# Optimization experiments

Hardware: AMD Instinct MI355X
Metric: run time of the kernel (lower is better)

## Reference

```python
import jax, jax.numpy as jnp
import numpy as np

T, OBS, H, NOBJ = 32768, 256, 512, 4


def _xavier(key, shape):
    fan_in, fan_out = shape[0], shape[1]
    lim = jnp.sqrt(6.0 / (fan_in + fan_out)).astype(jnp.float32)
    return jax.random.uniform(key, shape, jnp.float32, -lim, lim)


def setup_inputs() -> dict:
    key = jax.random.key(0)
    ks = jax.random.split(key, 16)
    # weights stored as [in, out] so y = x @ W (same math as nn.Linear with W.T)
    return {
        "x": jax.random.normal(ks[0], (T, OBS), jnp.float32),
        "W_in0": _xavier(ks[1], (OBS, H)),
        "W_B0": _xavier(ks[2], (OBS, H)),
        "W_C0": _xavier(ks[3], (OBS, H)),
        "W_d0": _xavier(ks[4], (OBS, H)),
        "A_log0": jax.random.normal(ks[5], (H,), jnp.float32),
        "W_in1": _xavier(ks[6], (H, H)),
        "W_B1": _xavier(ks[7], (H, H)),
        "W_C1": _xavier(ks[8], (H, H)),
        "W_d1": _xavier(ks[9], (H, H)),
        "A_log1": jax.random.normal(ks[10], (H,), jnp.float32),
        "W_out": _xavier(ks[11], (H, NOBJ)),
        "b_out": jnp.zeros((NOBJ,), jnp.float32),
        "W_skip": _xavier(ks[12], (OBS, NOBJ)),
    }


def _mamba_layer(x, W_in, W_B, W_C, W_d, A_log):
    # x: [T, D_in] -> [T, H]
    x_state = x @ W_in           # [T, H]
    B = x @ W_B                  # [T, H]
    C = x @ W_C                  # [T, H]
    delta = jax.nn.sigmoid(x @ W_d)  # [T, H]
    A = -jnp.exp(A_log)          # [H]
    A_bar = jnp.exp(delta * A)   # [T, H], in (0, 1)
    Bx = B * x_state             # [T, H]

    def step(h, inp):
        a_t, bx_t = inp
        h = a_t * h + bx_t
        return h, h

    h0 = jnp.zeros((x_state.shape[-1],), x_state.dtype)
    _, h_seq = jax.lax.scan(step, h0, (A_bar, Bx))  # [T, H]
    return C * h_seq


def reference(x, W_in0, W_B0, W_C0, W_d0, A_log0,
              W_in1, W_B1, W_C1, W_d1, A_log1,
              W_out, b_out, W_skip):
    skip = x
    y = _mamba_layer(x, W_in0, W_B0, W_C0, W_d0, A_log0)
    y = _mamba_layer(y, W_in1, W_B1, W_C1, W_d1, A_log1)
    out = y @ W_out + b_out + skip @ W_skip  # [T, NOBJ]
    return out
```

## Files before the change

### kernel.cpp

```cpp
#include <hip/hip_runtime.h>

typedef __attribute__((ext_vector_type(8))) short short8;
typedef __attribute__((ext_vector_type(4))) float floatx4;

#define T_SIZE 32768
#define OBS    256
#define H      512
#define NC     1024
#define CHUNK  32
#define NGRP   64
#define GCH    16
#define SLAB   ((size_t)T_SIZE * 32)

__device__ __forceinline__ unsigned short f2bf(float f){
    union { float f; unsigned u; } v; v.f = f;
    unsigned u = v.u;
    u += 0x7FFFu + ((u >> 16) & 1u);
    return (unsigned short)(u >> 16);
}
__device__ __forceinline__ float bf2f(unsigned short u){
    union { unsigned u; float f; } v; v.u = ((unsigned)u) << 16; return v.f;
}

#define GLOAD_LDS16(g, l) \
    __builtin_amdgcn_global_load_lds((const __attribute__((address_space(1))) unsigned*)(g), \
                                     (__attribute__((address_space(3))) unsigned*)(l), 16, 0, 0)

__global__ void cast_x_kernel(const float* __restrict__ x, unsigned short* __restrict__ xb, int n4){
    int i = blockIdx.x * 256 + threadIdx.x;
    if (i < n4){
        float4 v = ((const float4*)x)[i];
        ushort4 o;
        o.x = f2bf(v.x); o.y = f2bf(v.y); o.z = f2bf(v.z); o.w = f2bf(v.w);
        ((ushort4*)xb)[i] = o;
    }
}

__global__ void tcast4_kernel(const float* __restrict__ W0, const float* __restrict__ W1,
                              const float* __restrict__ W2, const float* __restrict__ W3,
                              unsigned short* __restrict__ dst, int K, int KH){
    int idx = blockIdx.x * 256 + threadIdx.x;
    if (idx >= 4 * KH) return;
    int s   = idx / KH;
    int rem = idx - s * KH;
    int k = rem >> 9;
    int h = rem & 511;
    const float* W = (s == 0) ? W0 : (s == 1) ? W1 : (s == 2) ? W2 : W3;
    int b = h >> 4, hh = h & 15;
    dst[(size_t)((b * 4 + s) * 16 + hh) * K + k] = f2bf(W[(size_t)k * H + h]);
}

template<int K>
__global__ __launch_bounds__(512, 2) void gemm_layer_kernel(
    const unsigned short* __restrict__ xb,
    const unsigned short* __restrict__ wt,
    const float* __restrict__ A_log,
    unsigned short* __restrict__ gT, unsigned short* __restrict__ bxT, unsigned short* __restrict__ CT,
    float* __restrict__ Pbuf, float* __restrict__ Hbuf)
{
    __shared__ unsigned short SM[4][16384];

    const int tid  = threadIdx.x;
    const int wave = tid >> 6;
    const int lane = tid & 63;
    const int ml   = lane & 15;
    const int quad = lane >> 4;
    const int wm   = wave >> 2;
    const int wn   = wave & 3;

    const int flat = blockIdx.y * 8 + blockIdx.x;
    const int xcd  = flat & 7;
    const int j    = flat >> 3;
    const int nb   = j & 7;
    const int mb   = (j >> 3) * 8 + xcd;
    const int m0   = mb * 256;

    const int srow = tid >> 2;
    const int sel  = ((tid & 3) ^ ((tid >> 3) & 3)) * 8;
    const int swz  = (ml >> 1) & 3;

    const unsigned short* pa0 = xb + (size_t)(m0 + srow) * K + sel;
    const unsigned short* pa1 = pa0 + (size_t)128 * K;
    const unsigned short* pb0 = wt + (size_t)(nb * 256 + srow) * K + sel;
    const unsigned short* pb1 = pb0 + (size_t)128 * K;

    const int ldsA0 = wave * 512;
    const int ldsA1 = 4096  + wave * 512;
    const int ldsB0 = 8192  + wave * 512;
    const int ldsB1 = 12288 + wave * 512;

    const int rbaseA = (wm * 128 + ml) * 32 + (quad ^ swz) * 8;
    const int rbaseB = (wn * 64  + ml) * 32 + (quad ^ swz) * 8;

    floatx4 acc[8][4];
    #pragma unroll
    for (int m = 0; m < 8; m++)
        #pragma unroll
        for (int n = 0; n < 4; n++)
            acc[m][n] = (floatx4)(0.0f);

    constexpr int NK = K >> 5;

#define STAGE_A(kt_) { const int b_ = (kt_) & 3; const int ko_ = (kt_) * 32; \
        GLOAD_LDS16(pa0 + ko_, &SM[b_][ldsA0]); \
        GLOAD_LDS16(pa1 + ko_, &SM[b_][ldsA1]); }
#define STAGE_B(kt_) { const int b_ = (kt_) & 3; const int ko_ = (kt_) * 32; \
        GLOAD_LDS16(pb0 + ko_, &SM[b_][ldsB0]); \
        GLOAD_LDS16(pb1 + ko_, &SM[b_][ldsB1]); }

    STAGE_A(0); STAGE_B(0);
    STAGE_A(1); STAGE_B(1);
    STAGE_A(2); STAGE_B(2);
    asm volatile("s_waitcnt vmcnt(8)" ::: "memory");
    __builtin_amdgcn_s_barrier();
    __builtin_amdgcn_sched_barrier(0);

    #pragma unroll
    for (int kt = 0; kt < NK; ++kt){
        const unsigned short* SA = &SM[kt & 3][0];
        const unsigned short* SB = SA + 8192;

        short8 av[4], bv[4];
        #pragma unroll
        for (int m = 0; m < 4; m++) av[m] = *(const short8*)(SA + rbaseA + m * 512);
        #pragma unroll
        for (int n = 0; n < 4; n++) bv[n] = *(const short8*)(SB + rbaseB + n * 512);
        if (kt + 3 < NK) STAGE_A(kt + 3);
        __builtin_amdgcn_s_barrier();
        asm volatile("s_waitcnt lgkmcnt(0)" ::: "memory");
        __builtin_amdgcn_sched_barrier(0);
        __builtin_amdgcn_s_setprio(1);
        #pragma unroll
        for (int m = 0; m < 4; m++)
            #pragma unroll
            for (int n = 0; n < 4; n++)
                acc[m][n] = __builtin_amdgcn_mfma_f32_16x16x32_bf16(av[m], bv[n], acc[m][n], 0, 0, 0);
        __builtin_amdgcn_s_setprio(0);
        __builtin_amdgcn_s_barrier();
        __builtin_amdgcn_sched_barrier(0);

        short8 aw[4];
        #pragma unroll
        for (int m = 0; m < 4; m++) aw[m] = *(const short8*)(SA + rbaseA + (m + 4) * 512);
        if (kt + 3 < NK) STAGE_B(kt + 3);
        __builtin_amdgcn_s_barrier();
        asm volatile("s_waitcnt lgkmcnt(0)" ::: "memory");
        __builtin_amdgcn_sched_barrier(0);
        __builtin_amdgcn_s_setprio(1);
        #pragma unroll
        for (int m = 0; m < 4; m++)
            #pragma unroll
            for (int n = 0; n < 4; n++)
                acc[m + 4][n] = __builtin_amdgcn_mfma_f32_16x16x32_bf16(aw[m], bv[n], acc[m + 4][n], 0, 0, 0);
        __builtin_amdgcn_s_setprio(0);
        if (kt + 1 < NK){
            if (kt + 3 < NK)       { asm volatile("s_waitcnt vmcnt(8)" ::: "memory"); }
            else if (kt + 3 == NK) { asm volatile("s_waitcnt vmcnt(4)" ::: "memory"); }
            else                   { asm volatile("s_waitcnt vmcnt(0)" ::: "memory"); }
        }
        __builtin_amdgcn_s_barrier();
        __builtin_amdgcn_sched_barrier(0);
    }
    __syncthreads();

#undef STAGE_A
#undef STAGE_B

    unsigned short* SMe = &SM[0][0];
    float2* segbuf = (float2*)(SMe + 49152);
    const int hcol  = wn * 16 + ml;
    const int hb    = wn >> 1;
    const int col32 = (wn & 1) * 16 + ml;
    const float Aneg = -expf(A_log[(nb * 4 + wn) * 16 + ml]);

    #pragma unroll
    for (int m = 0; m < 8; m++){
        float p = 1.0f, hh = 0.0f;
        #pragma unroll
        for (int r = 0; r < 4; r++){
            int trow = wm * 128 + m * 16 + quad * 4 + r;
            float dv = acc[m][3][r];
            float delta = 1.0f / (1.0f + expf(-dv));
            unsigned short gb = f2bf(delta * Aneg);
            float a = expf(bf2f(gb));
            unsigned short bb = f2bf(acc[m][1][r] * acc[m][0][r]);
            int base = hb * 8192 + trow * 32 + col32;
            SMe[        base] = gb;
            SMe[16384 + base] = bb;
            SMe[32768 + base] = f2bf(acc[m][2][r]);
            hh = fmaf(a, hh, bf2f(bb));
            p *= a;
        }
        const int ch = wm * 4 + (m >> 1);
        const int s  = (m & 1) * 4 + quad;
        segbuf[(ch * 8 + s) * 64 + hcol] = make_float2(p, hh);
    }
    __syncthreads();
    {
        const short8* s8 = (const short8*)SMe;
        #pragma unroll
        for (int arr = 0; arr < 3; arr++){
            unsigned short* bp = (arr == 0) ? gT : (arr == 1) ? bxT : CT;
            #pragma unroll
            for (int h2 = 0; h2 < 2; h2++){
                short8* d = (short8*)(bp + (size_t)(nb * 2 + h2) * SLAB + (size_t)m0 * 32);
                d[tid]       = s8[arr * 2048 + h2 * 1024 + tid];
                d[tid + 512] = s8[arr * 2048 + h2 * 1024 + tid + 512];
            }
        }
    }
    {
        const int ccol = tid & 63, ch = tid >> 6;
        float P = 1.0f, Hc = 0.0f;
        #pragma unroll
        for (int s = 0; s < 8; s++){
            float2 ph = segbuf[(ch * 8 + s) * 64 + ccol];
            Hc = fmaf(ph.x, Hc, ph.y);
            P *= ph.x;
        }
        const int c = mb * 8 + ch;
        Pbuf[(size_t)c * H + nb * 64 + ccol] = P;
        Hbuf[(size_t)c * H + nb * 64 + ccol] = Hc;
    }
}

__global__ void scan2a_kernel(const float* __restrict__ P, const float* __restrict__ Hc,
                              float* __restrict__ Pg, float* __restrict__ Hg){
    const int g  = blockIdx.x;
    const int j4 = threadIdx.x * 4;
    float4 pc = {1.f,1.f,1.f,1.f}, hc = {0.f,0.f,0.f,0.f};
    #pragma unroll
    for (int i = 0; i < GCH; i++){
        size_t o = (size_t)(g * GCH + i) * H + j4;
        float4 P4 = *(const float4*)(P + o);
        float4 H4 = *(const float4*)(Hc + o);
        hc.x = fmaf(P4.x, hc.x, H4.x); pc.x *= P4.x;
        hc.y = fmaf(P4.y, hc.y, H4.y); pc.y *= P4.y;
        hc.z = fmaf(P4.z, hc.z, H4.z); pc.z *= P4.z;
        hc.w = fmaf(P4.w, hc.w, H4.w); pc.w *= P4.w;
    }
    *(float4*)(Pg + (size_t)g * H + j4) = pc;
    *(float4*)(Hg + (size_t)g * H + j4) = hc;
}

__global__ void scan2b_kernel(const float* __restrict__ Pg, const float* __restrict__ Hg,
                              float* __restrict__ Cg){
    const int j = threadIdx.x;
    float carry = 0.0f;
    for (int g0 = 0; g0 < NGRP; g0 += 8){
        float p[8], h[8];
        #pragma unroll
        for (int i = 0; i < 8; i++){
            p[i] = Pg[(size_t)(g0 + i) * H + j];
            h[i] = Hg[(size_t)(g0 + i) * H + j];
        }
        #pragma unroll
        for (int i = 0; i < 8; i++){
            Cg[(size_t)(g0 + i) * H + j] = carry;
            carry = fmaf(p[i], carry, h[i]);
        }
    }
}

__global__ void scan3_kernel(const unsigned short* __restrict__ gT, const unsigned short* __restrict__ bxT,
                             const unsigned short* __restrict__ CT,
                             const float* __restrict__ P, const float* __restrict__ Hc,
                             const float* __restrict__ Cg,
                             unsigned short* __restrict__ yb){
    int idx = blockIdx.x * 256 + threadIdx.x;
    int j4 = (idx & 127) * 4;
    int c  = idx >> 7;
    int nb = j4 >> 5, jj = j4 & 31;
    int grp = c >> 4;
    float4 h = *(const float4*)(Cg + (size_t)grp * H + j4);
    for (int cc = grp << 4; cc < c; ++cc){
        float4 P4 = *(const float4*)(P + (size_t)cc * H + j4);
        float4 H4 = *(const float4*)(Hc + (size_t)cc * H + j4);
        h.x = fmaf(P4.x, h.x, H4.x);
        h.y = fmaf(P4.y, h.y, H4.y);
        h.z = fmaf(P4.z, h.z, H4.z);
        h.w = fmaf(P4.w, h.w, H4.w);
    }
    size_t off = (size_t)nb * SLAB + (size_t)c * CHUNK * 32 + jj;
    size_t yo  = (size_t)c * CHUNK * H + j4;
    #pragma unroll 8
    for (int i = 0; i < CHUNK; i++){
        ushort4 gv = *(const ushort4*)(gT + off);
        ushort4 bv = *(const ushort4*)(bxT + off);
        ushort4 cv = *(const ushort4*)(CT + off);
        h.x = fmaf(expf(bf2f(gv.x)), h.x, bf2f(bv.x));
        h.y = fmaf(expf(bf2f(gv.y)), h.y, bf2f(bv.y));
        h.z = fmaf(expf(bf2f(gv.z)), h.z, bf2f(bv.z));
        h.w = fmaf(expf(bf2f(gv.w)), h.w, bf2f(bv.w));
        ushort4 o;
        o.x = f2bf(bf2f(cv.x) * h.x);
        o.y = f2bf(bf2f(cv.y) * h.y);
        o.z = f2bf(bf2f(cv.z) * h.z);
        o.w = f2bf(bf2f(cv.w) * h.w);
        *(ushort4*)(yb + yo) = o;
        off += 32; yo += H;
    }
}

__global__ __launch_bounds__(256) void final_kernel(const unsigned short* __restrict__ y2,
                                                    const unsigned short* __restrict__ xb,
                                                    const float* __restrict__ Wout,
                                                    const float* __restrict__ bout,
                                                    const float* __restrict__ Wskip,
                                                    float* __restrict__ out){
    int wave = threadIdx.x >> 6;
    int lane = threadIdx.x & 63;
    int t = blockIdx.x * 4 + wave;
    float s0 = 0.f, s1 = 0.f, s2 = 0.f, s3 = 0.f;
    const float4* W4 = (const float4*)Wout;
    #pragma unroll
    for (int k = lane; k < H; k += 64){
        float yv = bf2f(y2[(size_t)t * H + k]);
        float4 w = W4[k];
        s0 = fmaf(yv, w.x, s0); s1 = fmaf(yv, w.y, s1);
        s2 = fmaf(yv, w.z, s2); s3 = fmaf(yv, w.w, s3);
    }
    const float4* S4 = (const float4*)Wskip;
    #pragma unroll
    for (int k = lane; k < OBS; k += 64){
        float xv = bf2f(xb[(size_t)t * OBS + k]);
        float4 w = S4[k];
        s0 = fmaf(xv, w.x, s0); s1 = fmaf(xv, w.y, s1);
        s2 = fmaf(xv, w.z, s2); s3 = fmaf(xv, w.w, s3);
    }
    #pragma unroll
    for (int off = 32; off > 0; off >>= 1){
        s0 += __shfl_down(s0, off);
        s1 += __shfl_down(s1, off);
        s2 += __shfl_down(s2, off);
        s3 += __shfl_down(s3, off);
    }
    if (lane == 0){
        out[(size_t)t * 4 + 0] = s0 + bout[0];
        out[(size_t)t * 4 + 1] = s1 + bout[1];
        out[(size_t)t * 4 + 2] = s2 + bout[2];
        out[(size_t)t * 4 + 3] = s3 + bout[3];
    }
}

extern "C" void kernel_launch(void* const* d_in, const int* in_sizes, int n_in,
                              void* d_out, int out_size, void* d_ws, size_t ws_size,
                              hipStream_t stream)
{
    const float* x     = (const float*)d_in[0];
    const float* W_in0 = (const float*)d_in[1];
    const float* W_B0  = (const float*)d_in[2];
    const float* W_C0  = (const float*)d_in[3];
    const float* W_d0  = (const float*)d_in[4];
    const float* A0    = (const float*)d_in[5];
    const float* W_in1 = (const float*)d_in[6];
    const float* W_B1  = (const float*)d_in[7];
    const float* W_C1  = (const float*)d_in[8];
    const float* W_d1  = (const float*)d_in[9];
    const float* A1    = (const float*)d_in[10];
    const float* Wout  = (const float*)d_in[11];
    const float* bout  = (const float*)d_in[12];
    const float* Wskip = (const float*)d_in[13];
    float* out = (float*)d_out;

    char* ws = (char*)d_ws;
    size_t off = 0;
    auto alloc = [&](size_t bytes) -> void* {
        void* p = ws + off;
        off += (bytes + 255) & ~(size_t)255;
        return p;
    };
    unsigned short* xb  = (unsigned short*)alloc((size_t)T_SIZE * OBS * 2);
    unsigned short* yb  = (unsigned short*)alloc((size_t)T_SIZE * H * 2);
    unsigned short* Wt0 = (unsigned short*)alloc((size_t)4 * H * OBS * 2);
    unsigned short* Wt1 = (unsigned short*)alloc((size_t)4 * H * H * 2);
    unsigned short* gT  = (unsigned short*)alloc((size_t)T_SIZE * H * 2);
    unsigned short* bxT = (unsigned short*)alloc((size_t)T_SIZE * H * 2);
    unsigned short* CT  = (unsigned short*)alloc((size_t)T_SIZE * H * 2);
    float* Pbuf = (float*)alloc((size_t)NC * H * 4);
    float* Hbuf = (float*)alloc((size_t)NC * H * 4);
    float* Pg   = (float*)alloc((size_t)NGRP * H * 4);
    float* Hg   = (float*)alloc((size_t)NGRP * H * 4);
    float* Cg   = (float*)alloc((size_t)NGRP * H * 4);
    (void)ws_size; (void)in_sizes; (void)n_in; (void)out_size;

    cast_x_kernel<<<(T_SIZE * OBS / 4 + 255) / 256, 256, 0, stream>>>(x, xb, T_SIZE * OBS / 4);
    tcast4_kernel<<<(4 * OBS * H + 255) / 256, 256, 0, stream>>>(W_in0, W_B0, W_C0, W_d0, Wt0, OBS, OBS * H);
    tcast4_kernel<<<(4 * H   * H + 255) / 256, 256, 0, stream>>>(W_in1, W_B1, W_C1, W_d1, Wt1, H,   H * H);

    dim3 ggrid(8, 128);
    const int sgrid = NC * 128 / 256;

    gemm_layer_kernel<OBS><<<ggrid, 512, 0, stream>>>(xb, Wt0, A0, gT, bxT, CT, Pbuf, Hbuf);
    scan2a_kernel<<<NGRP, 128, 0, stream>>>(Pbuf, Hbuf, Pg, Hg);
    scan2b_kernel<<<1, H, 0, stream>>>(Pg, Hg, Cg);
    scan3_kernel<<<sgrid, 256, 0, stream>>>(gT, bxT, CT, Pbuf, Hbuf, Cg, yb);

    gemm_layer_kernel<H><<<ggrid, 512, 0, stream>>>(yb, Wt1, A1, gT, bxT, CT, Pbuf, Hbuf);
    scan2a_kernel<<<NGRP, 128, 0, stream>>>(Pbuf, Hbuf, Pg, Hg);
    scan2b_kernel<<<1, H, 0, stream>>>(Pg, Hg, Cg);
    scan3_kernel<<<sgrid, 256, 0, stream>>>(gT, bxT, CT, Pbuf, Hbuf, Cg, yb );

    final_kernel<<<T_SIZE / 4, 256, 0, stream>>>(yb, xb, Wout, bout, Wskip, out);
}
```

Measured before the change: 336.0 us.

## Fuse chunked scan into GEMM epilogue with decoupled look-back across blocks

```diff
diff --git a/kernel.cpp b/kernel.cpp
--- a/kernel.cpp
+++ b/kernel.cpp
@@ -6,11 +6,8 @@
 #define T_SIZE 32768
 #define OBS    256
 #define H      512
-#define NC     1024
-#define CHUNK  32
-#define NGRP   64
-#define GCH    16
-#define SLAB   ((size_t)T_SIZE * 32)
+#define NBLK   8
+#define MBLK   128
 
 __device__ __forceinline__ unsigned short f2bf(float f){
     union { float f; unsigned u; } v; v.f = f;
@@ -51,14 +48,16 @@
 }
 
 template<int K>
-__global__ __launch_bounds__(512, 2) void gemm_layer_kernel(
+__global__ __launch_bounds__(512, 1) void gemm_layer_kernel(
     const unsigned short* __restrict__ xb,
     const unsigned short* __restrict__ wt,
     const float* __restrict__ A_log,
-    unsigned short* __restrict__ gT, unsigned short* __restrict__ bxT, unsigned short* __restrict__ CT,
-    float* __restrict__ Pbuf, float* __restrict__ Hbuf)
+    unsigned short* __restrict__ y,
+    float* __restrict__ AggP, float* __restrict__ AggH, float* __restrict__ Pref,
+    unsigned int* status)
 {
     __shared__ unsigned short SM[4][16384];
+    __shared__ float hp[64];
 
     const int tid  = threadIdx.x;
     const int wave = tid >> 6;
@@ -167,138 +166,119 @@
 #undef STAGE_B
 
     unsigned short* SMe = &SM[0][0];
-    float2* segbuf = (float2*)(SMe + 49152);
-    const int hcol  = wn * 16 + ml;
-    const int hb    = wn >> 1;
-    const int col32 = (wn & 1) * 16 + ml;
+    float2* segbuf = (float2*)SMe;
+    unsigned short* ystage = SMe + 32768;
+
+    const int hcol = wn * 16 + ml;
     const float Aneg = -expf(A_log[(nb * 4 + wn) * 16 + ml]);
 
+    unsigned gpk[16], bpk[16], cpk[16];
     #pragma unroll
     for (int m = 0; m < 8; m++){
         float p = 1.0f, hh = 0.0f;
         #pragma unroll
         for (int r = 0; r < 4; r++){
-            int trow = wm * 128 + m * 16 + quad * 4 + r;
             float dv = acc[m][3][r];
             float delta = 1.0f / (1.0f + expf(-dv));
             unsigned short gb = f2bf(delta * Aneg);
             float a = expf(bf2f(gb));
             unsigned short bb = f2bf(acc[m][1][r] * acc[m][0][r]);
-            int base = hb * 8192 + trow * 32 + col32;
-            SMe[        base] = gb;
-            SMe[16384 + base] = bb;
-            SMe[32768 + base] = f2bf(acc[m][2][r]);
+            unsigned short cb = f2bf(acc[m][2][r]);
+            if ((r & 1) == 0){
+                gpk[m*2 + (r>>1)] = (unsigned)gb;
+                bpk[m*2 + (r>>1)] = (unsigned)bb;
+                cpk[m*2 + (r>>1)] = (unsigned)cb;
+            } else {
+                gpk[m*2 + (r>>1)] |= ((unsigned)gb) << 16;
+                bpk[m*2 + (r>>1)] |= ((unsigned)bb) << 16;
+                cpk[m*2 + (r>>1)] |= ((unsigned)cb) << 16;
+            }
             hh = fmaf(a, hh, bf2f(bb));
             p *= a;
         }
-        const int ch = wm * 4 + (m >> 1);
-        const int s  = (m & 1) * 4 + quad;
-        segbuf[(ch * 8 + s) * 64 + hcol] = make_float2(p, hh);
+        const int sidx = wm * 32 + m * 4 + quad;
+        segbuf[sidx * 64 + hcol] = make_float2(p, hh);
     }
     __syncthreads();
+
+    if (tid < 64){
+        float P = 1.0f, Hh = 0.0f;
+        for (int s = 0; s < 64; s++){
+            float2 ph = segbuf[s * 64 + tid];
+            segbuf[s * 64 + tid] = make_float2(P, Hh);
+            Hh = fmaf(ph.x, Hh, ph.y);
+            P *= ph.x;
+        }
+        const size_t base = ((size_t)nb * MBLK + mb) * 64;
+        AggP[base + tid] = P;
+        AggH[base + tid] = Hh;
+        __threadfence();
+        if (tid == 0)
+            __hip_atomic_store(&status[nb * MBLK + mb], 1u, __ATOMIC_RELEASE, __HIP_MEMORY_SCOPE_AGENT);
+
+        float hin = 0.0f;
+        if (mb > 0){
+            float Pc = 1.0f, Hc = 0.0f;
+            int jj = mb - 1;
+            for (;;){
+                unsigned st;
+                do {
+                    st = __hip_atomic_load(&status[nb * MBLK + jj], __ATOMIC_ACQUIRE, __HIP_MEMORY_SCOPE_AGENT);
+                    st = __builtin_amdgcn_readfirstlane(st);
+                    if (st == 0u) __builtin_amdgcn_s_sleep(1);
+                } while (st == 0u);
+                const size_t bj = ((size_t)nb * MBLK + jj) * 64;
+                if (st == 2u){
+                    float pf = Pref[bj + tid];
+                    hin = fmaf(Pc, pf, Hc);
+                    break;
+                } else {
+                    float pj = AggP[bj + tid];
+                    float hj = AggH[bj + tid];
+                    Hc = fmaf(Pc, hj, Hc);
+                    Pc *= pj;
+                    if (--jj < 0){ hin = Hc; break; }
+                }
+            }
+        }
+        float hout = fmaf(P, hin, Hh);
+        Pref[base + tid] = hout;
+        __threadfence();
+        if (tid == 0)
+            __hip_atomic_store(&status[nb * MBLK + mb], 2u, __ATOMIC_RELEASE, __HIP_MEMORY_SCOPE_AGENT);
+        hp[tid] = hin;
+    }
+    __syncthreads();
+
     {
-        const short8* s8 = (const short8*)SMe;
-        #pragma unroll
-        for (int arr = 0; arr < 3; arr++){
-            unsigned short* bp = (arr == 0) ? gT : (arr == 1) ? bxT : CT;
+        const float hin_b = hp[hcol];
+        #pragma unroll
+        for (int m = 0; m < 8; m++){
+            const int sidx = wm * 32 + m * 4 + quad;
+            float2 pp = segbuf[sidx * 64 + hcol];
+            float h = fmaf(pp.x, hin_b, pp.y);
             #pragma unroll
-            for (int h2 = 0; h2 < 2; h2++){
-                short8* d = (short8*)(bp + (size_t)(nb * 2 + h2) * SLAB + (size_t)m0 * 32);
-                d[tid]       = s8[arr * 2048 + h2 * 1024 + tid];
-                d[tid + 512] = s8[arr * 2048 + h2 * 1024 + tid + 512];
+            for (int r = 0; r < 4; r++){
+                unsigned short gb = (unsigned short)((gpk[m*2 + (r>>1)] >> ((r & 1) * 16)) & 0xFFFFu);
+                unsigned short bb = (unsigned short)((bpk[m*2 + (r>>1)] >> ((r & 1) * 16)) & 0xFFFFu);
+                unsigned short cb = (unsigned short)((cpk[m*2 + (r>>1)] >> ((r & 1) * 16)) & 0xFFFFu);
+                float a = expf(bf2f(gb));
+                h = fmaf(a, h, bf2f(bb));
+                const int trow = wm * 128 + m * 16 + quad * 4 + r;
+                ystage[trow * 64 + hcol] = f2bf(bf2f(cb) * h);
             }
         }
     }
+    __syncthreads();
+
     {
-        const int ccol = tid & 63, ch = tid >> 6;
-        float P = 1.0f, Hc = 0.0f;
-        #pragma unroll
-        for (int s = 0; s < 8; s++){
-            float2 ph = segbuf[(ch * 8 + s) * 64 + ccol];
-            Hc = fmaf(ph.x, Hc, ph.y);
-            P *= ph.x;
-        }
-        const int c = mb * 8 + ch;
-        Pbuf[(size_t)c * H + nb * 64 + ccol] = P;
-        Hbuf[(size_t)c * H + nb * 64 + ccol] = Hc;
-    }
-}
-
-__global__ void scan2a_kernel(const float* __restrict__ P, const float* __restrict__ Hc,
-                              float* __restrict__ Pg, float* __restrict__ Hg){
-    const int g  = blockIdx.x;
-    const int j4 = threadIdx.x * 4;
-    float4 pc = {1.f,1.f,1.f,1.f}, hc = {0.f,0.f,0.f,0.f};
-    #pragma unroll
-    for (int i = 0; i < GCH; i++){
-        size_t o = (size_t)(g * GCH + i) * H + j4;
-        float4 P4 = *(const float4*)(P + o);
-        float4 H4 = *(const float4*)(Hc + o);
-        hc.x = fmaf(P4.x, hc.x, H4.x); pc.x *= P4.x;
-        hc.y = fmaf(P4.y, hc.y, H4.y); pc.y *= P4.y;
-        hc.z = fmaf(P4.z, hc.z, H4.z); pc.z *= P4.z;
-        hc.w = fmaf(P4.w, hc.w, H4.w); pc.w *= P4.w;
-    }
-    *(float4*)(Pg + (size_t)g * H + j4) = pc;
-    *(float4*)(Hg + (size_t)g * H + j4) = hc;
-}
-
-__global__ void scan2b_kernel(const float* __restrict__ Pg, const float* __restrict__ Hg,
-                              float* __restrict__ Cg){
-    const int j = threadIdx.x;
-    float carry = 0.0f;
-    for (int g0 = 0; g0 < NGRP; g0 += 8){
-        float p[8], h[8];
-        #pragma unroll
-        for (int i = 0; i < 8; i++){
-            p[i] = Pg[(size_t)(g0 + i) * H + j];
-            h[i] = Hg[(size_t)(g0 + i) * H + j];
-        }
-        #pragma unroll
-        for (int i = 0; i < 8; i++){
-            Cg[(size_t)(g0 + i) * H + j] = carry;
-            carry = fmaf(p[i], carry, h[i]);
-        }
-    }
-}
-
-__global__ void scan3_kernel(const unsigned short* __restrict__ gT, const unsigned short* __restrict__ bxT,
-                             const unsigned short* __restrict__ CT,
-                             const float* __restrict__ P, const float* __restrict__ Hc,
-                             const float* __restrict__ Cg,
-                             unsigned short* __restrict__ yb){
-    int idx = blockIdx.x * 256 + threadIdx.x;
-    int j4 = (idx & 127) * 4;
-    int c  = idx >> 7;
-    int nb = j4 >> 5, jj = j4 & 31;
-    int grp = c >> 4;
-    float4 h = *(const float4*)(Cg + (size_t)grp * H + j4);
-    for (int cc = grp << 4; cc < c; ++cc){
-        float4 P4 = *(const float4*)(P + (size_t)cc * H + j4);
-        float4 H4 = *(const float4*)(Hc + (size_t)cc * H + j4);
-        h.x = fmaf(P4.x, h.x, H4.x);
-        h.y = fmaf(P4.y, h.y, H4.y);
-        h.z = fmaf(P4.z, h.z, H4.z);
-        h.w = fmaf(P4.w, h.w, H4.w);
-    }
-    size_t off = (size_t)nb * SLAB + (size_t)c * CHUNK * 32 + jj;
-    size_t yo  = (size_t)c * CHUNK * H + j4;
-    #pragma unroll 8
-    for (int i = 0; i < CHUNK; i++){
-        ushort4 gv = *(const ushort4*)(gT + off);
-        ushort4 bv = *(const ushort4*)(bxT + off);
-        ushort4 cv = *(const ushort4*)(CT + off);
-        h.x = fmaf(expf(bf2f(gv.x)), h.x, bf2f(bv.x));
-        h.y = fmaf(expf(bf2f(gv.y)), h.y, bf2f(bv.y));
-        h.z = fmaf(expf(bf2f(gv.z)), h.z, bf2f(bv.z));
-        h.w = fmaf(expf(bf2f(gv.w)), h.w, bf2f(bv.w));
-        ushort4 o;
-        o.x = f2bf(bf2f(cv.x) * h.x);
-        o.y = f2bf(bf2f(cv.y) * h.y);
-        o.z = f2bf(bf2f(cv.z) * h.z);
-        o.w = f2bf(bf2f(cv.w) * h.w);
-        *(ushort4*)(yb + yo) = o;
-        off += 32; yo += H;
+        const short8* ys8 = (const short8*)ystage;
+        #pragma unroll
+        for (int k = 0; k < 4; k++){
+            int idx = k * 512 + tid;
+            int row = idx >> 3, c8 = idx & 7;
+            *(short8*)(y + (size_t)(m0 + row) * H + nb * 64 + c8 * 8) = ys8[idx];
+        }
     }
 }
 
@@ -371,35 +351,28 @@
         return p;
     };
     unsigned short* xb  = (unsigned short*)alloc((size_t)T_SIZE * OBS * 2);
-    unsigned short* yb  = (unsigned short*)alloc((size_t)T_SIZE * H * 2);
+    unsigned short* y0  = (unsigned short*)alloc((size_t)T_SIZE * H * 2);
+    unsigned short* y1  = (unsigned short*)alloc((size_t)T_SIZE * H * 2);
     unsigned short* Wt0 = (unsigned short*)alloc((size_t)4 * H * OBS * 2);
     unsigned short* Wt1 = (unsigned short*)alloc((size_t)4 * H * H * 2);
-    unsigned short* gT  = (unsigned short*)alloc((size_t)T_SIZE * H * 2);
-    unsigned short* bxT = (unsigned short*)alloc((size_t)T_SIZE * H * 2);
-    unsigned short* CT  = (unsigned short*)alloc((size_t)T_SIZE * H * 2);
-    float* Pbuf = (float*)alloc((size_t)NC * H * 4);
-    float* Hbuf = (float*)alloc((size_t)NC * H * 4);
-    float* Pg   = (float*)alloc((size_t)NGRP * H * 4);
-    float* Hg   = (float*)alloc((size_t)NGRP * H * 4);
-    float* Cg   = (float*)alloc((size_t)NGRP * H * 4);
+    float* AggP = (float*)alloc((size_t)NBLK * MBLK * 64 * 4);
+    float* AggH = (float*)alloc((size_t)NBLK * MBLK * 64 * 4);
+    float* Pref = (float*)alloc((size_t)NBLK * MBLK * 64 * 4);
+    unsigned int* st0 = (unsigned int*)alloc((size_t)NBLK * MBLK * 4);
+    unsigned int* st1 = (unsigned int*)alloc((size_t)NBLK * MBLK * 4);
     (void)ws_size; (void)in_sizes; (void)n_in; (void)out_size;
+
+    hipMemsetAsync(st0, 0, (size_t)NBLK * MBLK * 4 * 2, stream);
 
     cast_x_kernel<<<(T_SIZE * OBS / 4 + 255) / 256, 256, 0, stream>>>(x, xb, T_SIZE * OBS / 4);
     tcast4_kernel<<<(4 * OBS * H + 255) / 256, 256, 0, stream>>>(W_in0, W_B0, W_C0, W_d0, Wt0, OBS, OBS * H);
     tcast4_kernel<<<(4 * H   * H + 255) / 256, 256, 0, stream>>>(W_in1, W_B1, W_C1, W_d1, Wt1, H,   H * H);
 
     dim3 ggrid(8, 128);
-    const int sgrid = NC * 128 / 256;
-
-    gemm_layer_kernel<OBS><<<ggrid, 512, 0, stream>>>(xb, Wt0, A0, gT, bxT, CT, Pbuf, Hbuf);
-    scan2a_kernel<<<NGRP, 128, 0, stream>>>(Pbuf, Hbuf, Pg, Hg);
-    scan2b_kernel<<<1, H, 0, stream>>>(Pg, Hg, Cg);
-    scan3_kernel<<<sgrid, 256, 0, stream>>>(gT, bxT, CT, Pbuf, Hbuf, Cg, yb);
-
-    gemm_layer_kernel<H><<<ggrid, 512, 0, stream>>>(yb, Wt1, A1, gT, bxT, CT, Pbuf, Hbuf);
-    scan2a_kernel<<<NGRP, 128, 0, stream>>>(Pbuf, Hbuf, Pg, Hg);
-    scan2b_kernel<<<1, H, 0, stream>>>(Pg, Hg, Cg);
-    scan3_kernel<<<sgrid, 256, 0, stream>>>(gT, bxT, CT, Pbuf, Hbuf, Cg, yb );
-
-    final_kernel<<<T_SIZE / 4, 256, 0, stream>>>(yb, xb, Wout, bout, Wskip, out);
-}
+
+    gemm_layer_kernel<OBS><<<ggrid, 512, 0, stream>>>(xb, Wt0, A0, y0, AggP, AggH, Pref, st0);
+
+    gemm_layer_kernel<H><<<ggrid, 512, 0, stream>>>(y0, Wt1, A1, y1, AggP, AggH, Pref, st1);
+
+    final_kernel<<<T_SIZE / 4, 256, 0, stream>>>(y1, xb, Wout, bout, Wskip, out);
+}
```

After: 536.2 us. +59.6%, slower.
